# Kernel tuning notes

Measured on AMD Instinct MI355X. Metric: run time of the kernel, lower is better.

## Reference

```python
import jax, jax.numpy as jnp
import numpy as np

N = 500          # max_neurons, all alive
INPUT_SIZE = 3072
FEAT_DIM = 64
OUT_SIZE = 10
BATCH = 8192
RADIUS = 20.0
VOL = 100.0      # cubic volume (100,100,100)
N_ITER = 3


def setup_inputs() -> dict:
    key = jax.random.key(0)
    k_x, k_pos, k_iw, k_f, k_ow = jax.random.split(key, 5)
    x = jax.random.normal(k_x, (BATCH, INPUT_SIZE), dtype=jnp.float32)
    # seed positions spread across the volume, roughly matching _init_seeds
    positions = jax.random.uniform(k_pos, (N, 3), dtype=jnp.float32) * 80.0 + 10.0
    input_weights = jax.random.normal(k_iw, (N, INPUT_SIZE), dtype=jnp.float32) * 0.02
    features = jax.random.normal(k_f, (N, FEAT_DIM), dtype=jnp.float32) * 0.1
    output_weights = jax.random.normal(k_ow, (N, OUT_SIZE), dtype=jnp.float32) * 0.02
    biases = jnp.zeros((N,), dtype=jnp.float32)
    return {"x": x, "positions": positions, "input_weights": input_weights,
            "features": features, "output_weights": output_weights, "biases": biases}


def reference(x, positions, input_weights, features, output_weights, biases):
    # clamp positions into the volume (per-axis, vol is cubic here)
    pos = jnp.clip(positions, 0.1, VOL - 0.1)  # [N,3]

    # pairwise distances (grad-safe sqrt at the zero diagonal)
    diff = pos[:, None, :] - pos[None, :, :]          # [N,N,3]
    sq = jnp.sum(diff * diff, axis=-1)                # [N,N]
    pos_mask = sq > 0.0
    dist = jnp.where(pos_mask, jnp.sqrt(jnp.where(pos_mask, sq, 1.0)), 0.0)

    conn_mask = (dist < RADIUS) & (dist > 0.0)
    attenuation = jnp.exp(-dist / RADIUS) * conn_mask.astype(dist.dtype)

    # feature similarity (F.normalize clamps the norm from below at eps)
    feat_norm = features / jnp.maximum(
        jnp.linalg.norm(features, axis=1, keepdims=True), 1e-6)
    feat_sim = jnp.clip(feat_norm @ feat_norm.T, -1.0, 1.0)  # [N,N]

    conn_w = attenuation * (0.5 + 0.5 * feat_sim)
    conn_w = conn_w / (jnp.sum(conn_w, axis=1, keepdims=True) + 1e-6)

    # input gating: neurons near x=0 receive input
    x_norm = pos[:, 0] / VOL                          # [N]
    input_weight = jnp.exp(-2.0 * x_norm)
    input_weight = input_weight / (jnp.sum(input_weight) + 1e-6)

    activations = x @ input_weights.T * input_weight + biases  # [B,N]

    # iterative message passing (fixed small iteration count)
    for _ in range(N_ITER):
        msg = activations @ conn_w.T                  # [B,N]
        activations = jnp.minimum(jax.nn.relu(activations + 0.5 * msg), 50.0)

    # output gating: neurons near x=VOL emit output
    output_weight = jnp.exp(2.0 * (x_norm - 1.0))
    output_weight = output_weight / (jnp.sum(output_weight) + 1e-6)

    return activations @ (output_weights * output_weight[:, None])  # [B,OUT]
```

## Files before the change

kernel.cpp:

```cpp
#include <hip/hip_runtime.h>
#include <stdint.h>

#define N_REAL 500
#define NPAD   512
#define K_IN   3072
#define NBATCH 8192
#define NOUT   10
#define RADIUS 20.0f
#define VOLF   100.0f

typedef __attribute__((ext_vector_type(8))) __bf16 bf16x8;
typedef __attribute__((ext_vector_type(4))) float  f32x4;
typedef __attribute__((ext_vector_type(4))) unsigned short us4;

__device__ __forceinline__ unsigned short f2bf(float f) {
    unsigned int u = __float_as_uint(f);
    u += 0x7FFFu + ((u >> 16) & 1u);
    return (unsigned short)(u >> 16);
}
__device__ __forceinline__ float bf2f(unsigned short h) {
    return __uint_as_float(((unsigned int)h) << 16);
}
__device__ __forceinline__ uint2 cvt_pk4(float4 v) {
    uint2 r;
    asm("v_cvt_pk_bf16_f32 %0, %1, %2" : "=v"(r.x) : "v"(v.x), "v"(v.y));
    asm("v_cvt_pk_bf16_f32 %0, %1, %2" : "=v"(r.y) : "v"(v.z), "v"(v.w));
    return r;
}

#define GLOBAL_AS __attribute__((address_space(1)))
#define LDS_AS    __attribute__((address_space(3)))
__device__ __forceinline__ void glds16(const void* g, void* l) {
    __builtin_amdgcn_global_load_lds((const GLOBAL_AS void*)g, (LDS_AS void*)l, 16, 0, 0);
}

__global__ void prep1(const float* __restrict__ positions,
                      const float* __restrict__ features,
                      const float* __restrict__ out_w,
                      const float* __restrict__ biases,
                      float* __restrict__ feat_norm,
                      float* __restrict__ pos_c,
                      float* __restrict__ inw,
                      float* __restrict__ biasp,
                      float* __restrict__ wout)
{
    int n = threadIdx.x;
    float e_in = 0.f, e_out = 0.f;
    float px = 0.f, py = 0.f, pz = 0.f;
    if (n < N_REAL) {
        px = fminf(fmaxf(positions[n*3+0], 0.1f), VOLF - 0.1f);
        py = fminf(fmaxf(positions[n*3+1], 0.1f), VOLF - 0.1f);
        pz = fminf(fmaxf(positions[n*3+2], 0.1f), VOLF - 0.1f);
        float xn = px / VOLF;
        e_in  = expf(-2.f * xn);
        e_out = expf(2.f * (xn - 1.f));
        float ss = 0.f;
        for (int f = 0; f < 64; ++f) { float v = features[n*64+f]; ss += v*v; }
        float nm = fmaxf(sqrtf(ss), 1e-6f);
        for (int f = 0; f < 64; ++f) feat_norm[n*64+f] = features[n*64+f] / nm;
    } else {
        for (int f = 0; f < 64; ++f) feat_norm[n*64+f] = 0.f;
    }
    pos_c[n*4+0] = px; pos_c[n*4+1] = py; pos_c[n*4+2] = pz; pos_c[n*4+3] = 0.f;

    __shared__ float s_in[512], s_out[512];
    s_in[n] = e_in; s_out[n] = e_out;
    __syncthreads();
    for (int s = 256; s > 0; s >>= 1) {
        if (n < s) { s_in[n] += s_in[n+s]; s_out[n] += s_out[n+s]; }
        __syncthreads();
    }
    float sum_in  = s_in[0]  + 1e-6f;
    float sum_out = s_out[0] + 1e-6f;

    inw[n]   = (n < N_REAL) ? (e_in / sum_in) : 0.f;
    biasp[n] = (n < N_REAL) ? biases[n] : 0.f;
    float wo = (n < N_REAL) ? (e_out / sum_out) : 0.f;
    for (int o = 0; o < NOUT; ++o)
        wout[n*NOUT + o] = (n < N_REAL) ? out_w[n*NOUT + o] * wo : 0.f;
}

__global__ void prep2(const float* __restrict__ pos_c,
                      const float* __restrict__ feat_norm,
                      unsigned short* __restrict__ conn_w)
{
    int i = blockIdx.x;
    int t = threadIdx.x;
    __shared__ float fi[64];
    __shared__ float spos[4];
    __shared__ float red[128];
    if (t < 64) fi[t] = feat_norm[i*64 + t];
    if (t < 4)  spos[t] = pos_c[i*4 + t];
    __syncthreads();

    float w[4];
    float part = 0.f;
    for (int jj = 0; jj < 4; ++jj) {
        int j = t + jj*128;
        float val = 0.f;
        if (i < N_REAL && j < N_REAL) {
            float dx = spos[0] - pos_c[j*4+0];
            float dy = spos[1] - pos_c[j*4+1];
            float dz = spos[2] - pos_c[j*4+2];
            float sq = dx*dx + dy*dy + dz*dz;
            if (sq > 0.f) {
                float dist = sqrtf(sq);
                if (dist < RADIUS) {
                    float att = expf(-dist / RADIUS);
                    float sim = 0.f;
                    const float4* fj = (const float4*)(feat_norm + j*64);
                    const float4* fi4 = (const float4*)fi;
                    #pragma unroll
                    for (int f = 0; f < 16; ++f) {
                        float4 a = fi4[f]; float4 b = fj[f];
                        sim += a.x*b.x + a.y*b.y + a.z*b.z + a.w*b.w;
                    }
                    sim = fminf(fmaxf(sim, -1.f), 1.f);
                    val = att * (0.5f + 0.5f*sim);
                }
            }
        }
        w[jj] = val; part += val;
    }
    red[t] = part;
    __syncthreads();
    for (int s = 64; s > 0; s >>= 1) {
        if (t < s) red[t] += red[t+s];
        __syncthreads();
    }
    float inv = 1.f / (red[0] + 1e-6f);
    for (int jj = 0; jj < 4; ++jj)
        conn_w[(long)i*NPAD + t + jj*128] = f2bf(w[jj] * inv);
}

__global__ void cast_pad(const float* __restrict__ src, unsigned short* __restrict__ dst,
                         long total_q, long src_q)
{
    long i = (long)blockIdx.x * blockDim.x + threadIdx.x;
    long stride = (long)gridDim.x * blockDim.x;
    for (; i < total_q; i += stride) {
        us4 o;
        if (i < src_q) {
            float4 v = ((const float4*)src)[i];
            o[0] = f2bf(v.x); o[1] = f2bf(v.y); o[2] = f2bf(v.z); o[3] = f2bf(v.w);
        } else {
            o[0] = 0; o[1] = 0; o[2] = 0; o[3] = 0;
        }
        ((us4*)dst)[i] = o;
    }
}

__device__ __forceinline__ void block_map_g1(int b, int& m0, int& n0, int& ks) {
    int xcd = b & 7, loc = b >> 3;
    m0 = (xcd*16 + (loc >> 3)) * 64;
    int rest = loc & 7;
    n0 = (rest & 3) * 128;
    ks = rest >> 2;
}
__device__ __forceinline__ void block_map_g2(int b, int& m0, int& n0) {
    int xcd = b & 7, loc = b >> 3;
    m0 = (xcd*16 + (loc >> 2)) * 64;
    n0 = (loc & 3) * 128;
}

__global__ __launch_bounds__(256, 4)
void gemm1s(const float* __restrict__ X,
            const unsigned short* __restrict__ B,
            float* __restrict__ Pf)
{
    __shared__ unsigned short As[64*64];
    __shared__ unsigned short Bs[128*64];

    const int tid  = threadIdx.x;
    const int lane = tid & 63;
    const int wave = tid >> 6;
    int m0, n0, ks; block_map_g1(blockIdx.x, m0, n0, ks);
    const int kbase = ks * (K_IN/2);
    const int wm = (wave >> 1) * 32;
    const int wn = (wave & 1) * 64;

    f32x4 acc[2][4];
    #pragma unroll
    for (int i = 0; i < 2; ++i)
        #pragma unroll
        for (int j = 0; j < 4; ++j)
            acc[i][j] = (f32x4){0.f,0.f,0.f,0.f};

    const float4* gA[4]; int lAo[4];
    #pragma unroll
    for (int s = 0; s < 4; ++s) {
        int f = tid + s*256;
        int row = f >> 4, c4 = f & 15;
        gA[s] = (const float4*)(X + (long)(m0 + row) * K_IN + kbase) + c4;
        lAo[s] = row*128 + ((c4*8) ^ ((row & 7) << 4));
    }
    const char* gB[4]; char* lB[4];
    #pragma unroll
    for (int s = 0; s < 4; ++s) {
        int o = tid*16 + s*4096;
        int row = o >> 7, d = o & 127;
        gB[s] = (const char*)B + (long)(n0 + row) * (K_IN*2) + kbase*2 + (d ^ ((row & 7) << 4));
        lB[s] = (char*)Bs + o;
    }

    for (int t = 0; t < 24; ++t) {
        __syncthreads();
        #pragma unroll
        for (int s = 0; s < 4; ++s) { glds16(gB[s], lB[s]); gB[s] += 128; }
        float4 v[4];
        #pragma unroll
        for (int s = 0; s < 4; ++s) { v[s] = gA[s][0]; gA[s] += 16; }
        #pragma unroll
        for (int s = 0; s < 4; ++s)
            *(uint2*)((char*)As + lAo[s]) = cvt_pk4(v[s]);
        asm volatile("s_waitcnt vmcnt(0) lgkmcnt(0)" ::: "memory");
        __syncthreads();

        #pragma unroll
        for (int kk = 0; kk < 2; ++kk) {
            const int cb = kk*64 + (lane >> 4) * 16;
            bf16x8 afr[2], bfr[4];
            #pragma unroll
            for (int i = 0; i < 2; ++i) {
                int r = wm + i*16 + (lane & 15);
                afr[i] = *(const bf16x8*)((const char*)As + r*128 + (cb ^ ((r & 7) << 4)));
            }
            #pragma unroll
            for (int j = 0; j < 4; ++j) {
                int r = wn + j*16 + (lane & 15);
                bfr[j] = *(const bf16x8*)((const char*)Bs + r*128 + (cb ^ ((r & 7) << 4)));
            }
            #pragma unroll
            for (int i = 0; i < 2; ++i)
                #pragma unroll
                for (int j = 0; j < 4; ++j)
                    acc[i][j] = __builtin_amdgcn_mfma_f32_16x16x32_bf16(afr[i], bfr[j], acc[i][j], 0, 0, 0);
        }
    }

    float* P = Pf + (long)ks * (NBATCH * (long)NPAD);
    const int mbase = m0 + wm + (lane >> 4) * 4;
    const int nbase = n0 + wn + (lane & 15);
    #pragma unroll
    for (int j = 0; j < 4; ++j) {
        const int n = nbase + j*16;
        #pragma unroll
        for (int i = 0; i < 2; ++i)
            #pragma unroll
            for (int r = 0; r < 4; ++r) {
                const long m = mbase + i*16 + r;
                P[m*NPAD + n] = acc[i][j][r];
            }
    }
}

__global__ __launch_bounds__(256)
void reduce_ep(const float* __restrict__ Pf,
               const float* __restrict__ inw,
               const float* __restrict__ biasp,
               unsigned short* __restrict__ act)
{
    const long TOTQ = (long)NBATCH * NPAD / 4;
    long i = (long)blockIdx.x * blockDim.x + threadIdx.x;
    long stride = (long)gridDim.x * blockDim.x;
    for (; i < TOTQ; i += stride) {
        float4 a = ((const float4*)Pf)[i];
        float4 b = ((const float4*)Pf)[i + TOTQ];
        int nq = (int)(i & 127);
        float4 w  = ((const float4*)inw)[nq];
        float4 bi = ((const float4*)biasp)[nq];
        us4 o;
        o[0] = f2bf((a.x + b.x) * w.x + bi.x);
        o[1] = f2bf((a.y + b.y) * w.y + bi.y);
        o[2] = f2bf((a.z + b.z) * w.z + bi.z);
        o[3] = f2bf((a.w + b.w) * w.w + bi.w);
        ((us4*)act)[i] = o;
    }
}

__global__ __launch_bounds__(256, 4)
void gemm2_pipe(const unsigned short* __restrict__ A,
                const unsigned short* __restrict__ B,
                unsigned short* __restrict__ Cbf,
                const unsigned short* __restrict__ actOld)
{
    constexpr int ABUF = 8192;
    constexpr int BBUF = 16384;
    __shared__ __align__(16) char lds[3*(ABUF+BBUF)];
    char* const Abase = lds;
    char* const Bbase = lds + 3*ABUF;

    const int tid  = threadIdx.x;
    const int lane = tid & 63;
    const int wave = tid >> 6;
    int m0, n0; block_map_g2(blockIdx.x, m0, n0);
    const int wm = (wave >> 1) * 32;
    const int wn = (wave & 1) * 64;

    f32x4 acc[2][4];
    #pragma unroll
    for (int i = 0; i < 2; ++i)
        #pragma unroll
        for (int j = 0; j < 4; ++j)
            acc[i][j] = (f32x4){0.f,0.f,0.f,0.f};

    const char* gB[4]; int lBo[4];
    #pragma unroll
    for (int s = 0; s < 4; ++s) {
        int o = tid*16 + s*4096;
        int row = o >> 7, d = o & 127;
        gB[s] = (const char*)B + (long)(n0 + row) * (NPAD*2) + (d ^ ((row & 7) << 4));
        lBo[s] = o;
    }
    const char* gA1[2]; int lAo1[2];
    #pragma unroll
    for (int s = 0; s < 2; ++s) {
        int o = tid*16 + s*4096;
        int row = o >> 7, d = o & 127;
        gA1[s] = (const char*)A + (long)(m0 + row) * (NPAD*2) + (d ^ ((row & 7) << 4));
        lAo1[s] = o;
    }

    const int NT = NPAD >> 6;

    #pragma unroll
    for (int s = 0; s < 2; ++s) { glds16(gA1[s], Abase + 0*ABUF + lAo1[s]); gA1[s] += 128; }
    #pragma unroll
    for (int s = 0; s < 4; ++s) { glds16(gB[s], Bbase + 0*BBUF + lBo[s]); gB[s] += 128; }
    #pragma unroll
    for (int s = 0; s < 2; ++s) { glds16(gA1[s], Abase + 1*ABUF + lAo1[s]); gA1[s] += 128; }
    #pragma unroll
    for (int s = 0; s < 4; ++s) { glds16(gB[s], Bbase + 1*BBUF + lBo[s]); gB[s] += 128; }

    int cur = 0;
    for (int t = 0; t < NT; ++t) {
        int fb = cur + 2; if (fb >= 3) fb -= 3;
        const bool more2 = (t + 2 < NT);
        const bool more1 = (t + 1 < NT);
        if (more2) {
            #pragma unroll
            for (int s = 0; s < 2; ++s) { glds16(gA1[s], Abase + fb*ABUF + lAo1[s]); gA1[s] += 128; }
            #pragma unroll
            for (int s = 0; s < 4; ++s) { glds16(gB[s], Bbase + fb*BBUF + lBo[s]); gB[s] += 128; }
            asm volatile("s_waitcnt vmcnt(12)" ::: "memory");
        } else if (more1) {
            asm volatile("s_waitcnt vmcnt(6)" ::: "memory");
        } else {
            asm volatile("s_waitcnt vmcnt(0)" ::: "memory");
        }
        __builtin_amdgcn_s_barrier();

        const char* Ab = Abase + cur*ABUF;
        const char* Bb = Bbase + cur*BBUF;
        #pragma unroll
        for (int kk = 0; kk < 2; ++kk) {
            const int cb = kk*64 + (lane >> 4) * 16;
            bf16x8 afr[2], bfr[4];
            #pragma unroll
            for (int i = 0; i < 2; ++i) {
                int r = wm + i*16 + (lane & 15);
                afr[i] = *(const bf16x8*)(Ab + r*128 + (cb ^ ((r & 7) << 4)));
            }
            #pragma unroll
            for (int j = 0; j < 4; ++j) {
                int r = wn + j*16 + (lane & 15);
                bfr[j] = *(const bf16x8*)(Bb + r*128 + (cb ^ ((r & 7) << 4)));
            }
            #pragma unroll
            for (int i = 0; i < 2; ++i)
                #pragma unroll
                for (int j = 0; j < 4; ++j)
                    acc[i][j] = __builtin_amdgcn_mfma_f32_16x16x32_bf16(afr[i], bfr[j], acc[i][j], 0, 0, 0);
        }
        __builtin_amdgcn_s_barrier();
        cur = (cur == 2) ? 0 : cur + 1;
    }

    const int mbase = m0 + wm + (lane >> 4) * 4;
    const int nbase = n0 + wn + (lane & 15);
    #pragma unroll
    for (int j = 0; j < 4; ++j) {
        const int n = nbase + j*16;
        #pragma unroll
        for (int i = 0; i < 2; ++i)
            #pragma unroll
            for (int r = 0; r < 4; ++r) {
                const long m = mbase + i*16 + r;
                float old = bf2f(actOld[m*NPAD + n]);
                float vv = fminf(fmaxf(old + 0.5f * acc[i][j][r], 0.f), 50.f);
                Cbf[m*NPAD + n] = f2bf(vv);
            }
    }
}

__global__ __launch_bounds__(256)
void out_gemm(const unsigned short* __restrict__ act,
              const float* __restrict__ wout,
              float* __restrict__ out)
{
    __shared__ float sw[NPAD * NOUT];
    const int tid = threadIdx.x;
    for (int i = tid; i < NPAD*NOUT; i += 256) sw[i] = wout[i];
    __syncthreads();

    const int lane = tid & 63;
    const int wv   = tid >> 6;
    const int row  = blockIdx.x * 4 + wv;

    const unsigned short* ap = act + (long)row * NPAD + lane * 8;
    us4 v0 = *(const us4*)(ap);
    us4 v1 = *(const us4*)(ap + 4);

    float p[NOUT];
    #pragma unroll
    for (int o = 0; o < NOUT; ++o) p[o] = 0.f;

    const int nb = lane * 8;
    #pragma unroll
    for (int e = 0; e < 8; ++e) {
        float a = bf2f(e < 4 ? v0[e] : v1[e-4]);
        const float* wr = &sw[(nb + e) * NOUT];
        #pragma unroll
        for (int o = 0; o < NOUT; ++o) p[o] += a * wr[o];
    }
    #pragma unroll
    for (int o = 0; o < NOUT; ++o) {
        float s = p[o];
        for (int d = 32; d > 0; d >>= 1) s += __shfl_down(s, d);
        if (lane == 0) out[(long)row * NOUT + o] = s;
    }
}

extern "C" void kernel_launch(void* const* d_in, const int* in_sizes, int n_in,
                              void* d_out, int out_size, void* d_ws, size_t ws_size,
                              hipStream_t stream)
{
    const float* x        = (const float*)d_in[0];
    const float* pos      = (const float*)d_in[1];
    const float* in_w     = (const float*)d_in[2];
    const float* feats    = (const float*)d_in[3];
    const float* out_w    = (const float*)d_in[4];
    const float* biases   = (const float*)d_in[5];
    float* out = (float*)d_out;

    char* ws = (char*)d_ws;
    unsigned short* iw_bf  = (unsigned short*)(ws);
    unsigned short* connw  = (unsigned short*)(ws + 3145728);
    unsigned short* act_a  = (unsigned short*)(ws + 3670016);
    unsigned short* act_b  = (unsigned short*)(ws + 12058624);
    float* feat_norm = (float*)(ws + 20447232);
    float* pos_c     = (float*)(ws + 20578304);
    float* inw       = (float*)(ws + 20586496);
    float* biasp     = (float*)(ws + 20588544);
    float* wout      = (float*)(ws + 20590592);
    float* partials  = (float*)(ws + 20611072);

    prep1<<<1, 512, 0, stream>>>(pos, feats, out_w, biases, feat_norm, pos_c, inw, biasp, wout);
    prep2<<<512, 128, 0, stream>>>(pos_c, feat_norm, connw);
    cast_pad<<<512, 256, 0, stream>>>(in_w, iw_bf, 393216L, 384000L);

    gemm1s<<<1024, 256, 0, stream>>>(x, iw_bf, partials);
    reduce_ep<<<2048, 256, 0, stream>>>(partials, inw, biasp, act_a);

    gemm2_pipe<<<512, 256, 0, stream>>>(act_a, connw, act_b, act_a);
    gemm2_pipe<<<512, 256, 0, stream>>>(act_b, connw, act_a, act_b);
    gemm2_pipe<<<512, 256, 0, stream>>>(act_a, connw, act_b, act_a);

    out_gemm<<<NBATCH/4, 256, 0, stream>>>(act_b, wout, out);
}
```

Baseline: 120.6 us.

## Rewrite input GEMM with triple-buffered async LDS loads and fused epilogue

```diff
diff --git a/kernel.cpp b/kernel.cpp
--- a/kernel.cpp
+++ b/kernel.cpp
@@ -21,11 +21,13 @@
 __device__ __forceinline__ float bf2f(unsigned short h) {
     return __uint_as_float(((unsigned int)h) << 16);
 }
-__device__ __forceinline__ uint2 cvt_pk4(float4 v) {
-    uint2 r;
-    asm("v_cvt_pk_bf16_f32 %0, %1, %2" : "=v"(r.x) : "v"(v.x), "v"(v.y));
-    asm("v_cvt_pk_bf16_f32 %0, %1, %2" : "=v"(r.y) : "v"(v.z), "v"(v.w));
-    return r;
+__device__ __forceinline__ bf16x8 cvt8(float4 lo, float4 hi) {
+    union { unsigned int u[4]; bf16x8 v; } x;
+    asm("v_cvt_pk_bf16_f32 %0, %1, %2" : "=v"(x.u[0]) : "v"(lo.x), "v"(lo.y));
+    asm("v_cvt_pk_bf16_f32 %0, %1, %2" : "=v"(x.u[1]) : "v"(lo.z), "v"(lo.w));
+    asm("v_cvt_pk_bf16_f32 %0, %1, %2" : "=v"(x.u[2]) : "v"(hi.x), "v"(hi.y));
+    asm("v_cvt_pk_bf16_f32 %0, %1, %2" : "=v"(x.u[3]) : "v"(hi.z), "v"(hi.w));
+    return x.v;
 }
 
 #define GLOBAL_AS __attribute__((address_space(1)))
@@ -150,12 +152,10 @@
     }
 }
 
-__device__ __forceinline__ void block_map_g1(int b, int& m0, int& n0, int& ks) {
+__device__ __forceinline__ void block_map_g1(int b, int& m0, int& n0) {
     int xcd = b & 7, loc = b >> 3;
-    m0 = (xcd*16 + (loc >> 3)) * 64;
-    int rest = loc & 7;
-    n0 = (rest & 3) * 128;
-    ks = rest >> 2;
+    m0 = (xcd*16 + (loc >> 1)) * 64;
+    n0 = (loc & 1) * 256;
 }
 __device__ __forceinline__ void block_map_g2(int b, int& m0, int& n0) {
     int xcd = b & 7, loc = b >> 3;
@@ -163,21 +163,23 @@
     n0 = (loc & 3) * 128;
 }
 
-__global__ __launch_bounds__(256, 4)
-void gemm1s(const float* __restrict__ X,
-            const unsigned short* __restrict__ B,
-            float* __restrict__ Pf)
-{
-    __shared__ unsigned short As[64*64];
-    __shared__ unsigned short Bs[128*64];
+__global__ __launch_bounds__(512)
+void gemm1_r7(const float* __restrict__ Xf,
+              const unsigned short* __restrict__ B,
+              unsigned short* __restrict__ Cbf,
+              const float* __restrict__ inw,
+              const float* __restrict__ biasp)
+{
+    constexpr int ABUF = 16384;
+    constexpr int BBUF = 32768;
+    __shared__ __align__(16) char lds[3*ABUF + 3*BBUF];
 
     const int tid  = threadIdx.x;
     const int lane = tid & 63;
     const int wave = tid >> 6;
-    int m0, n0, ks; block_map_g1(blockIdx.x, m0, n0, ks);
-    const int kbase = ks * (K_IN/2);
-    const int wm = (wave >> 1) * 32;
-    const int wn = (wave & 1) * 64;
+    int m0, n0; block_map_g1(blockIdx.x, m0, n0);
+    const int wm = (wave >> 2) * 32;
+    const int wn = (wave & 3) * 64;
 
     f32x4 acc[2][4];
     #pragma unroll
@@ -186,49 +188,68 @@
         for (int j = 0; j < 4; ++j)
             acc[i][j] = (f32x4){0.f,0.f,0.f,0.f};
 
-    const float4* gA[4]; int lAo[4];
+    const char* gB[4]; int lBo[4];
     #pragma unroll
     for (int s = 0; s < 4; ++s) {
-        int f = tid + s*256;
-        int row = f >> 4, c4 = f & 15;
-        gA[s] = (const float4*)(X + (long)(m0 + row) * K_IN + kbase) + c4;
-        lAo[s] = row*128 + ((c4*8) ^ ((row & 7) << 4));
-    }
-    const char* gB[4]; char* lB[4];
-    #pragma unroll
-    for (int s = 0; s < 4; ++s) {
-        int o = tid*16 + s*4096;
+        int o = tid*16 + s*8192;
         int row = o >> 7, d = o & 127;
-        gB[s] = (const char*)B + (long)(n0 + row) * (K_IN*2) + kbase*2 + (d ^ ((row & 7) << 4));
-        lB[s] = (char*)Bs + o;
-    }
-
-    for (int t = 0; t < 24; ++t) {
-        __syncthreads();
-        #pragma unroll
-        for (int s = 0; s < 4; ++s) { glds16(gB[s], lB[s]); gB[s] += 128; }
-        float4 v[4];
-        #pragma unroll
-        for (int s = 0; s < 4; ++s) { v[s] = gA[s][0]; gA[s] += 16; }
-        #pragma unroll
-        for (int s = 0; s < 4; ++s)
-            *(uint2*)((char*)As + lAo[s]) = cvt_pk4(v[s]);
-        asm volatile("s_waitcnt vmcnt(0) lgkmcnt(0)" ::: "memory");
-        __syncthreads();
-
+        gB[s] = (const char*)B + (long)(n0 + row) * (K_IN*2) + (d ^ ((row & 7) << 4));
+        lBo[s] = o;
+    }
+    const char* gA[2]; int lAo[2];
+    #pragma unroll
+    for (int s = 0; s < 2; ++s) {
+        int o = tid*16 + s*8192;
+        int row = o >> 8, slot = (o >> 4) & 15;
+        gA[s] = (const char*)Xf + (long)(m0 + row) * (K_IN*4) + ((slot ^ (row & 15)) << 4);
+        lAo[s] = o;
+    }
+
+    const int NT = K_IN >> 6;
+
+#define ISSUE_TILE(p)                                                          \
+    do {                                                                       \
+        glds16(gA[0], lds + (p)*ABUF + lAo[0]); gA[0] += 256;                  \
+        glds16(gA[1], lds + (p)*ABUF + lAo[1]); gA[1] += 256;                  \
+        glds16(gB[0], lds + 3*ABUF + (p)*BBUF + lBo[0]); gB[0] += 128;         \
+        glds16(gB[1], lds + 3*ABUF + (p)*BBUF + lBo[1]); gB[1] += 128;         \
+        glds16(gB[2], lds + 3*ABUF + (p)*BBUF + lBo[2]); gB[2] += 128;         \
+        glds16(gB[3], lds + 3*ABUF + (p)*BBUF + lBo[3]); gB[3] += 128;         \
+    } while (0)
+
+    ISSUE_TILE(0);
+    ISSUE_TILE(1);
+
+    int cur = 0;
+    for (int t = 0; t < NT; ++t) {
+        int p2 = cur + 2; if (p2 >= 3) p2 -= 3;
+        if (t + 2 < NT) {
+            ISSUE_TILE(p2);
+            asm volatile("s_waitcnt vmcnt(12)" ::: "memory");
+        } else if (t + 1 < NT) {
+            asm volatile("s_waitcnt vmcnt(6)" ::: "memory");
+        } else {
+            asm volatile("s_waitcnt vmcnt(0)" ::: "memory");
+        }
+        __builtin_amdgcn_s_barrier();
+
+        const char* Ab = lds + cur*ABUF;
+        const char* Bb = lds + 3*ABUF + cur*BBUF;
         #pragma unroll
         for (int kk = 0; kk < 2; ++kk) {
-            const int cb = kk*64 + (lane >> 4) * 16;
             bf16x8 afr[2], bfr[4];
             #pragma unroll
             for (int i = 0; i < 2; ++i) {
                 int r = wm + i*16 + (lane & 15);
-                afr[i] = *(const bf16x8*)((const char*)As + r*128 + (cb ^ ((r & 7) << 4)));
+                int s0 = kk*8 + (lane >> 4)*2;
+                float4 lo = *(const float4*)(Ab + r*256 + (((s0    ) ^ (r & 15)) << 4));
+                float4 hi = *(const float4*)(Ab + r*256 + (((s0 + 1) ^ (r & 15)) << 4));
+                afr[i] = cvt8(lo, hi);
             }
             #pragma unroll
             for (int j = 0; j < 4; ++j) {
                 int r = wn + j*16 + (lane & 15);
-                bfr[j] = *(const bf16x8*)((const char*)Bs + r*128 + (cb ^ ((r & 7) << 4)));
+                bfr[j] = *(const bf16x8*)(Bb + r*128 + ((kk*64 + (lane >> 4)*16) ^ ((r & 7) << 4)));
             }
             #pragma unroll
             for (int i = 0; i < 2; ++i)
@@ -236,45 +257,24 @@
                 for (int j = 0; j < 4; ++j)
                     acc[i][j] = __builtin_amdgcn_mfma_f32_16x16x32_bf16(afr[i], bfr[j], acc[i][j], 0, 0, 0);
         }
-    }
-
-    float* P = Pf + (long)ks * (NBATCH * (long)NPAD);
+        __builtin_amdgcn_s_barrier();
+        cur = (cur == 2) ? 0 : cur + 1;
+    }
+#undef ISSUE_TILE
+
     const int mbase = m0 + wm + (lane >> 4) * 4;
     const int nbase = n0 + wn + (lane & 15);
     #pragma unroll
     for (int j = 0; j < 4; ++j) {
         const int n = nbase + j*16;
+        const float win = inw[n], bia = biasp[n];
         #pragma unroll
         for (int i = 0; i < 2; ++i)
             #pragma unroll
             for (int r = 0; r < 4; ++r) {
                 const long m = mbase + i*16 + r;
-                P[m*NPAD + n] = acc[i][j][r];
-            }
-    }
-}
-
-__global__ __launch_bounds__(256)
-void reduce_ep(const float* __restrict__ Pf,
-               const float* __restrict__ inw,
-               const float* __restrict__ biasp,
-               unsigned short* __restrict__ act)
-{
-    const long TOTQ = (long)NBATCH * NPAD / 4;
-    long i = (long)blockIdx.x * blockDim.x + threadIdx.x;
-    long stride = (long)gridDim.x * blockDim.x;
-    for (; i < TOTQ; i += stride) {
-        float4 a = ((const float4*)Pf)[i];
-        float4 b = ((const float4*)Pf)[i + TOTQ];
-        int nq = (int)(i & 127);
-        float4 w  = ((const float4*)inw)[nq];
-        float4 bi = ((const float4*)biasp)[nq];
-        us4 o;
-        o[0] = f2bf((a.x + b.x) * w.x + bi.x);
-        o[1] = f2bf((a.y + b.y) * w.y + bi.y);
-        o[2] = f2bf((a.z + b.z) * w.z + bi.z);
-        o[3] = f2bf((a.w + b.w) * w.w + bi.w);
-        ((us4*)act)[i] = o;
+                Cbf[m*NPAD + n] = f2bf(acc[i][j][r] * win + bia);
+            }
     }
 }
 
@@ -453,14 +453,12 @@
     float* inw       = (float*)(ws + 20586496);
     float* biasp     = (float*)(ws + 20588544);
     float* wout      = (float*)(ws + 20590592);
-    float* partials  = (float*)(ws + 20611072);
 
     prep1<<<1, 512, 0, stream>>>(pos, feats, out_w, biases, feat_norm, pos_c, inw, biasp, wout);
     prep2<<<512, 128, 0, stream>>>(pos_c, feat_norm, connw);
     cast_pad<<<512, 256, 0, stream>>>(in_w, iw_bf, 393216L, 384000L);
 
-    gemm1s<<<1024, 256, 0, stream>>>(x, iw_bf, partials);
-    reduce_ep<<<2048, 256, 0, stream>>>(partials, inw, biasp, act_a);
+    gemm1_r7<<<256, 512, 0, stream>>>(x, iw_bf, act_a, inw, biasp);
 
     gemm2_pipe<<<512, 256, 0, stream>>>(act_a, connw, act_b, act_a);
     gemm2_pipe<<<512, 256, 0, stream>>>(act_b, connw, act_a, act_b);
```

Result: slower. 129.1 us (+7.0%).

## Drop split-K in input GEMM and fuse scale-bias epilogue into it

Applied to the files above, without the earlier changes.

```diff
diff --git a/kernel.cpp b/kernel.cpp
--- a/kernel.cpp
+++ b/kernel.cpp
@@ -150,23 +150,18 @@
     }
 }
 
-__device__ __forceinline__ void block_map_g1(int b, int& m0, int& n0, int& ks) {
-    int xcd = b & 7, loc = b >> 3;
-    m0 = (xcd*16 + (loc >> 3)) * 64;
-    int rest = loc & 7;
-    n0 = (rest & 3) * 128;
-    ks = rest >> 2;
-}
 __device__ __forceinline__ void block_map_g2(int b, int& m0, int& n0) {
     int xcd = b & 7, loc = b >> 3;
     m0 = (xcd*16 + (loc >> 2)) * 64;
     n0 = (loc & 3) * 128;
 }
 
-__global__ __launch_bounds__(256, 4)
-void gemm1s(const float* __restrict__ X,
-            const unsigned short* __restrict__ B,
-            float* __restrict__ Pf)
+__global__ __launch_bounds__(256)
+void gemm1_strict(const float* __restrict__ X,
+                  const unsigned short* __restrict__ B,
+                  unsigned short* __restrict__ Cbf,
+                  const float* __restrict__ inw,
+                  const float* __restrict__ biasp)
 {
     __shared__ unsigned short As[64*64];
     __shared__ unsigned short Bs[128*64];
@@ -174,8 +169,7 @@
     const int tid  = threadIdx.x;
     const int lane = tid & 63;
     const int wave = tid >> 6;
-    int m0, n0, ks; block_map_g1(blockIdx.x, m0, n0, ks);
-    const int kbase = ks * (K_IN/2);
+    int m0, n0; block_map_g2(blockIdx.x, m0, n0);
     const int wm = (wave >> 1) * 32;
     const int wn = (wave & 1) * 64;
 
@@ -191,7 +185,7 @@
     for (int s = 0; s < 4; ++s) {
         int f = tid + s*256;
         int row = f >> 4, c4 = f & 15;
-        gA[s] = (const float4*)(X + (long)(m0 + row) * K_IN + kbase) + c4;
+        gA[s] = (const float4*)(X + (long)(m0 + row) * K_IN) + c4;
         lAo[s] = row*128 + ((c4*8) ^ ((row & 7) << 4));
     }
     const char* gB[4]; char* lB[4];
@@ -199,11 +193,11 @@
     for (int s = 0; s < 4; ++s) {
         int o = tid*16 + s*4096;
         int row = o >> 7, d = o & 127;
-        gB[s] = (const char*)B + (long)(n0 + row) * (K_IN*2) + kbase*2 + (d ^ ((row & 7) << 4));
+        gB[s] = (const char*)B + (long)(n0 + row) * (K_IN*2) + (d ^ ((row & 7) << 4));
         lB[s] = (char*)Bs + o;
     }
 
-    for (int t = 0; t < 24; ++t) {
+    for (int t = 0; t < 48; ++t) {
         __syncthreads();
         #pragma unroll
         for (int s = 0; s < 4; ++s) { glds16(gB[s], lB[s]); gB[s] += 128; }
@@ -238,43 +232,19 @@
         }
     }
 
-    float* P = Pf + (long)ks * (NBATCH * (long)NPAD);
     const int mbase = m0 + wm + (lane >> 4) * 4;
     const int nbase = n0 + wn + (lane & 15);
     #pragma unroll
     for (int j = 0; j < 4; ++j) {
         const int n = nbase + j*16;
+        const float win = inw[n], bia = biasp[n];
         #pragma unroll
         for (int i = 0; i < 2; ++i)
             #pragma unroll
             for (int r = 0; r < 4; ++r) {
                 const long m = mbase + i*16 + r;
-                P[m*NPAD + n] = acc[i][j][r];
-            }
-    }
-}
-
-__global__ __launch_bounds__(256)
-void reduce_ep(const float* __restrict__ Pf,
-               const float* __restrict__ inw,
-               const float* __restrict__ biasp,
-               unsigned short* __restrict__ act)
-{
-    const long TOTQ = (long)NBATCH * NPAD / 4;
-    long i = (long)blockIdx.x * blockDim.x + threadIdx.x;
-    long stride = (long)gridDim.x * blockDim.x;
-    for (; i < TOTQ; i += stride) {
-        float4 a = ((const float4*)Pf)[i];
-        float4 b = ((const float4*)Pf)[i + TOTQ];
-        int nq = (int)(i & 127);
-        float4 w  = ((const float4*)inw)[nq];
-        float4 bi = ((const float4*)biasp)[nq];
-        us4 o;
-        o[0] = f2bf((a.x + b.x) * w.x + bi.x);
-        o[1] = f2bf((a.y + b.y) * w.y + bi.y);
-        o[2] = f2bf((a.z + b.z) * w.z + bi.z);
-        o[3] = f2bf((a.w + b.w) * w.w + bi.w);
-        ((us4*)act)[i] = o;
+                Cbf[m*NPAD + n] = f2bf(acc[i][j][r] * win + bia);
+            }
     }
 }
 
@@ -453,14 +423,12 @@
     float* inw       = (float*)(ws + 20586496);
     float* biasp     = (float*)(ws + 20588544);
     float* wout      = (float*)(ws + 20590592);
-    float* partials  = (float*)(ws + 20611072);
 
     prep1<<<1, 512, 0, stream>>>(pos, feats, out_w, biases, feat_norm, pos_c, inw, biasp, wout);
     prep2<<<512, 128, 0, stream>>>(pos_c, feat_norm, connw);
     cast_pad<<<512, 256, 0, stream>>>(in_w, iw_bf, 393216L, 384000L);
 
-    gemm1s<<<1024, 256, 0, stream>>>(x, iw_bf, partials);
-    reduce_ep<<<2048, 256, 0, stream>>>(partials, inw, biasp, act_a);
+    gemm1_strict<<<512, 256, 0, stream>>>(x, iw_bf, act_a, inw, biasp);
 
     gemm2_pipe<<<512, 256, 0, stream>>>(act_a, connw, act_b, act_a);
     gemm2_pipe<<<512, 256, 0, stream>>>(act_b, connw, act_a, act_b);
```

Result: faster. 116.1 us (-3.8%).
